# Kernel tuning notes

Hardware: AMD Instinct MI355X
Metric: run time of the kernel (lower is better)

Reference implementation:

```python
import jax, jax.numpy as jnp
import numpy as np

B_SZ, L, D_MODEL, D_STATE, D_CONV, EXPAND = 8, 2048, 512, 16, 4, 2
D_INNER = EXPAND * D_MODEL
DT_RANK = (D_MODEL + 15) // 16  # 32
ENC_IN, MARK_IN, C_OUT, PRED_LEN = 7, 4, 7, 96
IN_SIZE = ENC_IN + MARK_IN


def setup_inputs() -> dict:
    key = jax.random.key(0)
    ks = jax.random.split(key, 16)
    s = 0.02
    inp = {
        "x_enc": jax.random.normal(ks[0], (B_SZ, L, ENC_IN), jnp.float32),
        "x_mark_enc": jax.random.normal(ks[1], (B_SZ, L, MARK_IN), jnp.float32),
        "x_dec": jax.random.normal(ks[2], (B_SZ, PRED_LEN, ENC_IN), jnp.float32),
        "x_mark_dec": jax.random.normal(ks[3], (B_SZ, PRED_LEN, MARK_IN), jnp.float32),
        # input_transform
        "W_in": jax.random.normal(ks[4], (IN_SIZE, D_MODEL), jnp.float32) * s,
        "b_in": jnp.zeros((D_MODEL,), jnp.float32),
        # mamba in_proj (no bias)
        "W_inproj": jax.random.normal(ks[5], (D_MODEL, 2 * D_INNER), jnp.float32) * s,
        # depthwise causal conv
        "conv_w": jax.random.normal(ks[6], (D_INNER, D_CONV), jnp.float32) * s,
        "conv_b": jnp.zeros((D_INNER,), jnp.float32),
        # x_proj -> dt, B, C (no bias)
        "W_xproj": jax.random.normal(ks[7], (D_INNER, DT_RANK + 2 * D_STATE), jnp.float32) * s,
        # dt_proj
        "W_dt": jax.random.normal(ks[8], (DT_RANK, D_INNER), jnp.float32) * s,
        "b_dt": jnp.log(jnp.expm1(jnp.full((D_INNER,), 0.01, jnp.float32))),  # softplus-inv of ~0.01
        # S4D real init
        "A_log": jnp.log(jnp.broadcast_to(jnp.arange(1, D_STATE + 1, dtype=jnp.float32), (D_INNER, D_STATE))),
        "D": jnp.ones((D_INNER,), jnp.float32),
        # out_proj (no bias)
        "W_out": jax.random.normal(ks[9], (D_INNER, D_MODEL), jnp.float32) * s,
        # head
        "W_fc": jax.random.normal(ks[10], (D_MODEL, C_OUT), jnp.float32) * s,
        "b_fc": jnp.zeros((C_OUT,), jnp.float32),
    }
    return inp


def _mamba(x, W_inproj, conv_w, conv_b, W_xproj, W_dt, b_dt, A_log, D, W_out):
    # x: (B, L, d_model)
    xz = x @ W_inproj                      # (B, L, 2*d_inner)
    u, z = jnp.split(xz, 2, axis=-1)       # each (B, L, d_inner)
    # causal depthwise conv over time
    u_t = jnp.transpose(u, (0, 2, 1))      # (B, d_inner, L)
    conv = jax.lax.conv_general_dilated(
        u_t, conv_w[:, None, :], (1,), [(D_CONV - 1, 0)],
        dimension_numbers=("NCH", "OIH", "NCH"), feature_group_count=D_INNER)
    u = jax.nn.silu(jnp.transpose(conv, (0, 2, 1)) + conv_b)  # (B, L, d_inner)

    x_dbl = u @ W_xproj                    # (B, L, dt_rank + 2*d_state)
    dt_lo, Bmat, Cmat = jnp.split(x_dbl, [DT_RANK, DT_RANK + D_STATE], axis=-1)
    dt = jax.nn.softplus(dt_lo @ W_dt + b_dt)  # (B, L, d_inner)
    A = -jnp.exp(A_log)                    # (d_inner, d_state)

    def step(h, inp):
        dt_t, B_t, C_t, u_t = inp          # (B,d_inner),(B,d_state),(B,d_state),(B,d_inner)
        dA = jnp.exp(dt_t[:, :, None] * A)                       # (B, d_inner, d_state)
        dBu = dt_t[:, :, None] * B_t[:, None, :] * u_t[:, :, None]
        h = dA * h + dBu
        y = jnp.einsum("bds,bs->bd", h, C_t) + D * u_t
        return h, y

    h0 = jnp.zeros((x.shape[0], D_INNER, D_STATE), x.dtype)
    xs = (jnp.swapaxes(dt, 0, 1), jnp.swapaxes(Bmat, 0, 1),
          jnp.swapaxes(Cmat, 0, 1), jnp.swapaxes(u, 0, 1))
    _, ys = jax.lax.scan(step, h0, xs)     # ys: (L, B, d_inner)
    y = jnp.swapaxes(ys, 0, 1) * jax.nn.silu(z)
    return y @ W_out                       # (B, L, d_model)


def reference(x_enc, x_mark_enc, x_dec, x_mark_dec, W_in, b_in, W_inproj,
              conv_w, conv_b, W_xproj, W_dt, b_dt, A_log, D, W_out, W_fc, b_fc):
    x = jnp.concatenate([x_enc, x_mark_enc], axis=-1) @ W_in + b_in  # (B, L, d_model)
    x = _mamba(x, W_inproj, conv_w, conv_b, W_xproj, W_dt, b_dt, A_log, D, W_out)
    return x[:, -PRED_LEN:, :] @ W_fc + b_fc  # (B, pred_len, c_out)
```

## Files before the change

### kernel.cpp

```cpp
#include <hip/hip_runtime.h>
#include <math.h>

#define BB 8
#define LL 2048
#define DI 1024
#define NS 16
#define RK 32
#define NI 11
#define PRED 96
#define NC 7

static constexpr size_t OFF_WF   = 0;
static constexpr size_t OFF_BF   = 22528;
static constexpr size_t OFF_A2   = 24576;
static constexpr size_t OFF_WOF  = 40960;
static constexpr size_t OFF_CWT  = 48128;
static constexpr size_t OFF_WXH  = 52224;
static constexpr size_t OFF_WDTH = 84992;
static constexpr size_t OFF_BC   = 101376;
static constexpr size_t OFF_CC   = 363520;
static constexpr size_t OFF_YS   = 625664;
static constexpr size_t OFF_PB   = 1412096;
static constexpr size_t OFF_HB   = 5606400;
static constexpr size_t OFF_UH   = 9800704;
static constexpr size_t OFF_DT   = 18189312;
static constexpr size_t OFF_DLH  = 26577920;
static constexpr size_t OFF_PP   = OFF_PB;
static constexpr size_t OFF_PC   = OFF_PB + 196608;

typedef __attribute__((ext_vector_type(8))) __bf16 bf16x8;
typedef __attribute__((ext_vector_type(8))) _Float16 f16x8;
typedef __attribute__((ext_vector_type(4))) float f32x4;
typedef __attribute__((ext_vector_type(2))) float f32x2;

__device__ __forceinline__ float fexp2(float x) {
#if __has_builtin(__builtin_amdgcn_exp2f)
  return __builtin_amdgcn_exp2f(x);
#else
  return exp2f(x);
#endif
}
__device__ __forceinline__ unsigned short f2bf(float f) {
  unsigned int b = __float_as_uint(f);
  unsigned int r = (b + 0x7fffu + ((b >> 16) & 1u)) >> 16;
  return (unsigned short)r;
}
__device__ __forceinline__ unsigned short f2h_u(float f) {
  union { _Float16 h; unsigned short u; } c;
  c.h = (_Float16)f;
  return c.u;
}
__device__ __forceinline__ float h2f(unsigned short u) {
  union { unsigned short u; _Float16 h; } c;
  c.u = u;
  return (float)c.h;
}
__device__ __forceinline__ float softp(float a) {
  return (a > 15.f) ? a : __logf(1.f + __expf(a));
}
__device__ __forceinline__ f32x2 pk_mul(f32x2 a, f32x2 b) {
  f32x2 d;
  asm("v_pk_mul_f32 %0, %1, %2" : "=v"(d) : "v"(a), "v"(b));
  return d;
}
__device__ __forceinline__ f32x2 pk_fma(f32x2 a, f32x2 b, f32x2 c) {
  asm("v_pk_fma_f32 %0, %1, %2, %0" : "+v"(c) : "v"(a), "v"(b));
  return c;
}
__device__ __forceinline__ void pow16(float e1, float* p) {
  float c2 = e1 * e1, c4 = c2 * c2, c8 = c4 * c4;
  p[0] = e1; p[1] = c2; p[2] = c2 * e1; p[3] = c4;
  p[4] = c4 * e1; p[5] = c4 * c2; p[6] = c4 * p[2]; p[7] = c8;
#pragma unroll
  for (int j = 0; j < 8; ++j) p[8 + j] = c8 * p[j];
}

__global__ __launch_bounds__(256) void k_pre1(
    const float* __restrict__ W_in, const float* __restrict__ b_in,
    const float* __restrict__ W_inproj, const float* __restrict__ conv_w,
    const float* __restrict__ W_xproj, const float* __restrict__ W_dt,
    const float* __restrict__ A_log,
    const float* __restrict__ W_out, const float* __restrict__ W_fc,
    float* __restrict__ ws) {
  int bid = blockIdx.x, tid = threadIdx.x;
  if (bid < 768) {
    int ks = bid / 96;
    int out = (bid % 96) * 256 + tid;
    int r = out >> 11, c = out & 2047;
    int k0 = ks * 64;
    float acc = 0.f;
    for (int k = 0; k < 64; ++k) {
      float a = (r < NI) ? W_in[r * 512 + k0 + k] : b_in[k0 + k];
      acc = fmaf(a, W_inproj[(size_t)(k0 + k) * 2048 + c], acc);
    }
    ws[OFF_PP + (size_t)ks * 24576 + out] = acc;
  } else if (bid < 832) {
    int idx = (bid - 768) * 256 + tid;
    ws[OFF_A2 + idx] = -expf(A_log[idx]) * 1.4426950408889634f;
  } else if (bid < 1056) {
    int lb = bid - 832;
    int ks = lb / 28;
    int out = (lb % 28) * 256 + tid;
    int d = out / NC, cc = out - d * NC;
    int k0 = ks * 64;
    float acc = 0.f;
    for (int k = 0; k < 64; ++k)
      acc = fmaf(W_out[(size_t)d * 512 + k0 + k], W_fc[(k0 + k) * NC + cc], acc);
    ws[OFF_PC + (size_t)ks * 7168 + out] = acc;
  } else if (bid < 1072) {
    int idx = (bid - 1056) * 256 + tid;
    int k = idx >> 10, dd = idx & 1023;
    ws[OFF_CWT + idx] = conv_w[dd * 4 + k];
  } else if (bid < 1328) {
    int idx = (bid - 1072) * 256 + tid;
    int c = idx >> 10, k = idx & 1023;
    unsigned short* wxh = (unsigned short*)(ws + OFF_WXH);
    wxh[idx] = f2bf(W_xproj[(size_t)k * 64 + c]);
  } else {
    int idx = (bid - 1328) * 256 + tid;
    int dd = idx >> 5, k = idx & 31;
    unsigned short* wdh = (unsigned short*)(ws + OFF_WDTH);
    wdh[idx] = f2h_u(W_dt[(size_t)k * DI + dd]);
  }
}

__global__ __launch_bounds__(256) void k_pre2(float* __restrict__ ws) {
  int idx = blockIdx.x * 256 + threadIdx.x;
  if (idx < 24576) {
    float acc = 0.f;
    for (int ks = 0; ks < 8; ++ks) acc += ws[OFF_PP + (size_t)ks * 24576 + idx];
    int r = idx >> 11, c = idx & 2047;
    if (r < NI) ws[OFF_WF + (size_t)r * 2048 + c] = acc;
    else ws[OFF_BF + c] = acc;
  } else {
    int i2 = idx - 24576;
    float acc = 0.f;
    for (int ks = 0; ks < 8; ++ks) acc += ws[OFF_PC + (size_t)ks * 7168 + i2];
    ws[OFF_WOF + i2] = acc;
  }
}

__global__ __launch_bounds__(256) void k_u(
    const float* __restrict__ xe, const float* __restrict__ xm,
    const float* __restrict__ conv_b, float* __restrict__ ws) {
  __shared__ float scat[11][11];
  __shared__ unsigned short sld[8][264];
  int bid = blockIdx.x, tid = threadIdx.x;
  int tg = bid >> 2, dq = bid & 3;
  int d = dq * 256 + tid;
  int b = tg >> 8;
  int t0 = (tg & 255) * 8;
  if (tid < 121) {
    int k = tid / 11, i = tid - k * 11;
    int tp = t0 - 3 + k;
    float v = 0.f;
    if (tp >= 0) v = (i < 7) ? xe[(size_t)(b * LL + tp) * 7 + i]
                             : xm[(size_t)(b * LL + tp) * 4 + (i - 7)];
    scat[k][i] = v;
  }
  __syncthreads();
  float wfv[NI];
#pragma unroll
  for (int i = 0; i < NI; ++i) wfv[i] = ws[OFF_WF + (size_t)i * 2048 + d];
  float bfu = ws[OFF_BF + d];
  float cwv[4];
#pragma unroll
  for (int k = 0; k < 4; ++k) cwv[k] = ws[OFF_CWT + k * 1024 + d];
  float cbv = conv_b[d];
  float xzv[11];
#pragma unroll
  for (int w2 = 0; w2 < 11; ++w2) {
    int tp = t0 - 3 + w2;
    float xz = bfu;
#pragma unroll
    for (int i = 0; i < NI; ++i) xz = fmaf(scat[w2][i], wfv[i], xz);
    xzv[w2] = (tp >= 0) ? xz : 0.f;
  }
#pragma unroll
  for (int tt = 0; tt < 8; ++tt) {
    float acc = cbv;
#pragma unroll
    for (int k = 0; k < 4; ++k) acc = fmaf(cwv[k], xzv[tt + k], acc);
    float uval = acc / (1.f + __expf(-acc));
    sld[tt][tid] = f2bf(uval);
  }
  __syncthreads();
  unsigned short* uhp = (unsigned short*)(ws + OFF_UH);
  int row = tid >> 5, q = tid & 31;
  *(uint4*)(uhp + (size_t)(b * LL + t0 + row) * DI + dq * 256 + q * 8) =
      *(const uint4*)&sld[row][q * 8];
}

__global__ __launch_bounds__(256) void k_proj(float* __restrict__ ws) {
  __shared__ unsigned short su[32][72];
  __shared__ unsigned short sw[64][72];
  __shared__ unsigned short so_dl[32][32];
  __shared__ unsigned short so_b[32][16];
  __shared__ float so_c[32][16];
  const unsigned short* uh  = (const unsigned short*)(ws + OFF_UH);
  const unsigned short* wxh = (const unsigned short*)(ws + OFF_WXH);
  int bid = blockIdx.x, tid = threadIdx.x;
  int r0 = bid * 32;
  int lane = tid & 63, w = tid >> 6;
  int rt = w >> 1, cp = w & 1;
  int srow = tid >> 3, skg = tid & 7;
  const ushort* ub0 = uh + (size_t)(r0 + srow) * DI + skg * 8;
  const ushort* wb0 = wxh + (size_t)srow * DI + skg * 8;
  uint4 ru[2], rw[2][2];
  ru[0]    = *(const uint4*)(ub0);
  rw[0][0] = *(const uint4*)(wb0);
  rw[0][1] = *(const uint4*)(wb0 + (size_t)32 * DI);
  ru[1]    = *(const uint4*)(ub0 + 64);
  rw[1][0] = *(const uint4*)(wb0 + 64);
  rw[1][1] = *(const uint4*)(wb0 + (size_t)32 * DI + 64);
  f32x4 acc[2];
  acc[0] = (f32x4){0.f, 0.f, 0.f, 0.f};
  acc[1] = (f32x4){0.f, 0.f, 0.f, 0.f};
  int arow = rt * 16 + (lane & 15);
  for (int kt = 0; kt < 16; ++kt) {
    int set = kt & 1;
    __syncthreads();
    *(uint4*)&su[srow][skg * 8]      = ru[set];
    *(uint4*)&sw[srow][skg * 8]      = rw[set][0];
    *(uint4*)&sw[srow + 32][skg * 8] = rw[set][1];
    __syncthreads();
    if (kt + 2 < 16) {
      int ko = (kt + 2) * 64;
      ru[set]    = *(const uint4*)(ub0 + ko);
      rw[set][0] = *(const uint4*)(wb0 + ko);
      rw[set][1] = *(const uint4*)(wb0 + (size_t)32 * DI + ko);
    }
#pragma unroll
    for (int ks = 0; ks < 2; ++ks) {
      int koff = ks * 32 + (lane >> 4) * 8;
      bf16x8 av = *(const bf16x8*)&su[arow][koff];
#pragma unroll
      for (int nt = 0; nt < 2; ++nt) {
        bf16x8 bv = *(const bf16x8*)&sw[cp * 32 + nt * 16 + (lane & 15)][koff];
        acc[nt] = __builtin_amdgcn_mfma_f32_16x16x32_bf16(av, bv, acc[nt], 0, 0, 0);
      }
    }
  }
  int orow = rt * 16 + ((lane >> 4) << 2);
  int ocol = lane & 15;
  __syncthreads();
  if (cp == 0) {
#pragma unroll
    for (int reg = 0; reg < 4; ++reg) {
      so_dl[orow + reg][ocol]      = f2h_u(acc[0][reg]);
      so_dl[orow + reg][16 + ocol] = f2h_u(acc[1][reg]);
    }
  } else {
#pragma unroll
    for (int reg = 0; reg < 4; ++reg) {
      so_b[orow + reg][ocol] = f2h_u(acc[0][reg]);
      so_c[orow + reg][ocol] = acc[1][reg];
    }
  }
  __syncthreads();
  unsigned short* dlh = (unsigned short*)(ws + OFF_DLH);
  unsigned short* bh  = (unsigned short*)(ws + OFF_BC);
  if (tid < 128) {
    ((uint4*)(dlh + (size_t)r0 * 32))[tid] = ((const uint4*)so_dl)[tid];
  } else if (tid < 192) {
    int i = tid - 128;
    ((uint4*)(bh + (size_t)r0 * NS))[i] = ((const uint4*)so_b)[i];
  } else {
    int i = tid - 192;
    uint4* cdst = (uint4*)(ws + OFF_CC + (size_t)r0 * NS);
    cdst[i]      = ((const uint4*)so_c)[i];
    cdst[i + 64] = ((const uint4*)so_c)[i + 64];
  }
}

__global__ __launch_bounds__(256) void k_dt(
    const float* __restrict__ b_dt, float* __restrict__ ws) {
  __shared__ _Float16 sdl[64][44];
  __shared__ _Float16 swd[128][44];
  __shared__ unsigned short sst[64][136];
  const unsigned short* dlh = (const unsigned short*)(ws + OFF_DLH);
  const unsigned short* wdh = (const unsigned short*)(ws + OFF_WDTH);
  unsigned short* dtg = (unsigned short*)(ws + OFF_DT);
  int bid = blockIdx.x, tid = threadIdx.x;
  int tgrp = bid >> 3, dgrp = bid & 7;
  int t0 = tgrp * 64, d0 = dgrp * 128;
  {
    int row = tid >> 2, q = tid & 3;
    *(uint4*)&sdl[row][q * 8] = *(const uint4*)&dlh[(size_t)(t0 + row) * 32 + q * 8];
  }
#pragma unroll
  for (int j = 0; j < 2; ++j) {
    int i = j * 256 + tid, row = i >> 2, q = i & 3;
    *(uint4*)&swd[row][q * 8] = *(const uint4*)&wdh[(size_t)(d0 + row) * 32 + q * 8];
  }
  __syncthreads();
  int lane = tid & 63, w = tid >> 6;
  int cl = lane & 15, kg = lane >> 4;
  f16x8 af = *(const f16x8*)&sdl[w * 16 + cl][kg * 8];
#pragma unroll
  for (int dq = 0; dq < 8; ++dq) {
    f16x8 bf8 = *(const f16x8*)&swd[dq * 16 + cl][kg * 8];
    f32x4 a2 = (f32x4){0.f, 0.f, 0.f, 0.f};
    a2 = __builtin_amdgcn_mfma_f32_16x16x32_f16(af, bf8, a2, 0, 0, 0);
    float bdt = b_dt[d0 + dq * 16 + cl];
#pragma unroll
    for (int r = 0; r < 4; ++r)
      sst[w * 16 + kg * 4 + r][dq * 16 + cl] = f2h_u(softp(a2[r] + bdt));
  }
  __syncthreads();
#pragma unroll
  for (int j = 0; j < 4; ++j) {
    int i = j * 256 + tid, row = i >> 4, q = i & 15;
    *(uint4*)(dtg + (size_t)(t0 + row) * DI + d0 + q * 8) =
        *(const uint4*)&sst[row][q * 8];
  }
}

__global__ __launch_bounds__(128) void k_scan1(float* __restrict__ ws) {
  __shared__ float sBB[64][16];
  int ch = blockIdx.x, dgrp = blockIdx.y, b = blockIdx.z;
  int tid = threadIdx.x;
  int d0 = dgrp * 128, t0 = ch * 64;
  size_t row0 = (size_t)b * LL + t0;
  const unsigned short* uh  = (const unsigned short*)(ws + OFF_UH) + row0 * DI + d0 + tid;
  const unsigned short* dtg = (const unsigned short*)(ws + OFF_DT) + row0 * DI + d0 + tid;
  const unsigned short* Bh  = (const unsigned short*)(ws + OFF_BC) + row0 * NS;
  {
    int row = tid >> 1, q = tid & 1;
    uint4 raw = *(const uint4*)(Bh + (size_t)row * NS + q * 8);
    f16x8 hv = *(f16x8*)&raw;
    float4 f0 = {(float)hv[0], (float)hv[1], (float)hv[2], (float)hv[3]};
    float4 f1 = {(float)hv[4], (float)hv[5], (float)hv[6], (float)hv[7]};
    *(float4*)&sBB[row][q * 8]     = f0;
    *(float4*)&sBB[row][q * 8 + 4] = f1;
  }
  __syncthreads();
  int d = d0 + tid;
  float a20 = ws[OFF_A2 + (size_t)d * NS];
  f32x2 h2[8];
#pragma unroll
  for (int j = 0; j < 8; ++j) h2[j] = (f32x2){0.f, 0.f};
  float S = 0.f;
#pragma unroll 4
  for (int t = 0; t < 64; ++t) {
    float dtv = h2f(dtg[(size_t)t * DI]);
    float uv  = __uint_as_float((unsigned)uh[(size_t)t * DI] << 16);
    float dtu = dtv * uv;
    S += dtv;
    float e1 = fexp2(dtv * a20);
    float c2 = e1 * e1, c4 = c2 * c2, c8 = c4 * c4;
    f32x2 c4p = (f32x2){c4, c4}, c8p = (f32x2){c8, c8};
    f32x2 pr0 = (f32x2){e1, c2};
    f32x2 pr1 = pk_mul(pr0, (f32x2){c2, c2});
    f32x2 pr2 = pk_mul(pr0, c4p);
    f32x2 pr3 = pk_mul(pr1, c4p);
    f32x2 pr4 = pk_mul(pr0, c8p);
    f32x2 pr5 = pk_mul(pr1, c8p);
    f32x2 pr6 = pk_mul(pr2, c8p);
    f32x2 pr7 = pk_mul(pr3, c8p);
    f32x2 du2 = (f32x2){dtu, dtu};
    const f32x2* bp = (const f32x2*)&sBB[t][0];
    h2[0] = pk_fma(pr0, h2[0], pk_mul(bp[0], du2));
    h2[1] = pk_fma(pr1, h2[1], pk_mul(bp[1], du2));
    h2[2] = pk_fma(pr2, h2[2], pk_mul(bp[2], du2));
    h2[3] = pk_fma(pr3, h2[3], pk_mul(bp[3], du2));
    h2[4] = pk_fma(pr4, h2[4], pk_mul(bp[4], du2));
    h2[5] = pk_fma(pr5, h2[5], pk_mul(bp[5], du2));
    h2[6] = pk_fma(pr6, h2[6], pk_mul(bp[6], du2));
    h2[7] = pk_fma(pr7, h2[7], pk_mul(bp[7], du2));
  }
  float E1 = fexp2(S * a20);
  ws[OFF_PB + ((size_t)b * 32 + ch) * 1024 + d] = E1;
  unsigned short* hbh = (unsigned short*)(ws + OFF_HB);
  size_t hbase = (((size_t)b * 32 + ch) * NS) * 1024 + d;
#pragma unroll
  for (int s = 0; s < 16; ++s) {
    float hv = (s & 1) ? h2[s >> 1].y : h2[s >> 1].x;
    hbh[hbase + (size_t)s * 1024] = f2h_u(hv);
  }
}

__global__ __launch_bounds__(128) void k_tail(
    const float* __restrict__ Dvec, float* __restrict__ ws) {
  __shared__ unsigned short sdt[64][128];
  __shared__ unsigned short suu[64][128];
  __shared__ float sBB[64][16];
  __shared__ float sCC[64][16];
  int bid = blockIdx.x, tid = threadIdx.x;
  int b = bid >> 4, dgrp = (bid >> 1) & 7, half = bid & 1;
  int d0 = dgrp * 128, t0 = (30 + half) * 64;
  size_t row0 = (size_t)b * LL + t0;
  const unsigned short* uh  = (const unsigned short*)(ws + OFF_UH) + row0 * DI + d0;
  const unsigned short* dtg = (const unsigned short*)(ws + OFF_DT) + row0 * DI + d0;
  const unsigned short* Bh  = (const unsigned short*)(ws + OFF_BC) + row0 * NS;
  const float* Cp = ws + OFF_CC + row0 * NS;
#pragma unroll
  for (int j = 0; j < 8; ++j) {
    int i = j * 128 + tid, row = i >> 4, q = i & 15;
    *(uint4*)&suu[row][q * 8] = *(const uint4*)(uh + (size_t)row * DI + q * 8);
    *(uint4*)&sdt[row][q * 8] = *(const uint4*)(dtg + (size_t)row * DI + q * 8);
  }
#pragma unroll
  for (int j = 0; j < 2; ++j) {
    int i = j * 128 + tid, row = i >> 2, q = i & 3;
    *(float4*)&sCC[row][q * 4] = *(const float4*)&Cp[(size_t)row * NS + q * 4];
  }
  {
    int row = tid >> 1, q = tid & 1;
    uint4 raw = *(const uint4*)(Bh + (size_t)row * NS + q * 8);
    f16x8 hv = *(f16x8*)&raw;
    float4 f0 = {(float)hv[0], (float)hv[1], (float)hv[2], (float)hv[3]};
    float4 f1 = {(float)hv[4], (float)hv[5], (float)hv[6], (float)hv[7]};
    *(float4*)&sBB[row][q * 8]     = f0;
    *(float4*)&sBB[row][q * 8 + 4] = f1;
  }
  int d = d0 + tid;
  float h[16];
#pragma unroll
  for (int s = 0; s < 16; ++s) h[s] = 0.f;
  const unsigned short* hbh = (const unsigned short*)(ws + OFF_HB);
  int nch = 30 + half;
  for (int c = 0; c < nch; ++c) {
    float E1c = ws[OFF_PB + ((size_t)b * 32 + c) * 1024 + d];
    float P[16];
    pow16(E1c, P);
    size_t cb = (((size_t)b * 32 + c) * NS) * 1024 + d;
#pragma unroll
    for (int s = 0; s < 16; ++s)
      h[s] = fmaf(P[s], h[s], h2f(hbh[cb + (size_t)s * 1024]));
  }
  __syncthreads();
  float a20 = ws[OFF_A2 + (size_t)d * NS];
  float Dv = Dvec[d];
  float* ysp = ws + OFF_YS;
  int tstart = half ? 0 : 32;
  for (int t = 0; t < 64; ++t) {
    float dtv = h2f(sdt[t][tid]);
    float uv  = __uint_as_float((unsigned)suu[t][tid] << 16);
    float dtu = dtv * uv;
    float e1 = fexp2(dtv * a20);
    float p[16];
    pow16(e1, p);
    f32x4 b0 = *(const f32x4*)&sBB[t][0];
    f32x4 b1 = *(const f32x4*)&sBB[t][4];
    f32x4 b2 = *(const f32x4*)&sBB[t][8];
    f32x4 b3 = *(const f32x4*)&sBB[t][12];
#pragma unroll
    for (int j = 0; j < 4; ++j) {
      h[j]      = fmaf(p[j],      h[j],      b0[j] * dtu);
      h[j + 4]  = fmaf(p[j + 4],  h[j + 4],  b1[j] * dtu);
      h[j + 8]  = fmaf(p[j + 8],  h[j + 8],  b2[j] * dtu);
      h[j + 12] = fmaf(p[j + 12], h[j + 12], b3[j] * dtu);
    }
    if (t >= tstart) {
      f32x4 c0 = *(const f32x4*)&sCC[t][0];
      f32x4 c1 = *(const f32x4*)&sCC[t][4];
      f32x4 c2 = *(const f32x4*)&sCC[t][8];
      f32x4 c3 = *(const f32x4*)&sCC[t][12];
      float pv = h[0] * c0[0] + h[1] * c0[1] + h[2] * c0[2] + h[3] * c0[3]
               + h[4] * c1[0] + h[5] * c1[1] + h[6] * c1[2] + h[7] * c1[3]
               + h[8] * c2[0] + h[9] * c2[1] + h[10] * c2[2] + h[11] * c2[3]
               + h[12] * c3[0] + h[13] * c3[1] + h[14] * c3[2] + h[15] * c3[3];
      ysp[((size_t)(b * PRED + (t0 + t - (LL - PRED)))) * DI + d] = fmaf(Dv, uv, pv);
    }
  }
}

__global__ __launch_bounds__(256) void k_out(
    const float* __restrict__ xe, const float* __restrict__ xm,
    const float* __restrict__ b_fc, const float* __restrict__ ws,
    float* __restrict__ out) {
  __shared__ float scat[NI];
  __shared__ float sacc[4][NC];
  int bid = blockIdx.x, tid = threadIdx.x;
  int b = bid / PRED, p = bid - b * PRED;
  int t = LL - PRED + p;
  if (tid < NI) scat[tid] = (tid < 7) ? xe[(size_t)(b * LL + t) * 7 + tid]
                                      : xm[(size_t)(b * LL + t) * 4 + (tid - 7)];
  __syncthreads();
  const float* Wf  = ws + OFF_WF;
  const float* bf  = ws + OFF_BF;
  const float* Wof = ws + OFF_WOF;
  const float* ysp = ws + OFF_YS + ((size_t)bid) * DI;
  float acc[NC];
#pragma unroll
  for (int cc = 0; cc < NC; ++cc) acc[cc] = 0.f;
#pragma unroll
  for (int j = 0; j < 4; ++j) {
    int dd = tid + j * 256;
    float zv = bf[DI + dd];
#pragma unroll
    for (int i = 0; i < NI; ++i) zv = fmaf(scat[i], Wf[(size_t)i * 2048 + DI + dd], zv);
    float g = ysp[dd] * (zv / (1.f + __expf(-zv)));
#pragma unroll
    for (int cc = 0; cc < NC; ++cc) acc[cc] = fmaf(g, Wof[dd * NC + cc], acc[cc]);
  }
#pragma unroll
  for (int cc = 0; cc < NC; ++cc) {
    float v = acc[cc];
    for (int off = 32; off > 0; off >>= 1) v += __shfl_down(v, off);
    if ((tid & 63) == 0) sacc[tid >> 6][cc] = v;
  }
  __syncthreads();
  if (tid < NC)
    out[(size_t)bid * NC + tid] =
        sacc[0][tid] + sacc[1][tid] + sacc[2][tid] + sacc[3][tid] + b_fc[tid];
}

extern "C" void kernel_launch(void* const* d_in, const int* in_sizes, int n_in,
                              void* d_out, int out_size, void* d_ws, size_t ws_size,
                              hipStream_t stream) {
  const float* xe    = (const float*)d_in[0];
  const float* xm    = (const float*)d_in[1];
  const float* W_in  = (const float*)d_in[4];
  const float* b_in  = (const float*)d_in[5];
  const float* W_ip  = (const float*)d_in[6];
  const float* cw    = (const float*)d_in[7];
  const float* cb    = (const float*)d_in[8];
  const float* W_xp  = (const float*)d_in[9];
  const float* W_dt  = (const float*)d_in[10];
  const float* b_dt  = (const float*)d_in[11];
  const float* A_log = (const float*)d_in[12];
  const float* Dv    = (const float*)d_in[13];
  const float* W_out = (const float*)d_in[14];
  const float* W_fc  = (const float*)d_in[15];
  const float* b_fc  = (const float*)d_in[16];
  float* ws  = (float*)d_ws;
  float* out = (float*)d_out;

  k_pre1 <<<1456, 256, 0, stream>>>(W_in, b_in, W_ip, cw, W_xp, W_dt, A_log, W_out, W_fc, ws);
  k_pre2 <<<124, 256, 0, stream>>>(ws);
  k_u    <<<8192, 256, 0, stream>>>(xe, xm, cb, ws);
  k_proj <<<512, 256, 0, stream>>>(ws);
  k_dt   <<<2048, 256, 0, stream>>>(b_dt, ws);
  k_scan1<<<dim3(31, 8, 8), 128, 0, stream>>>(ws);
  k_tail <<<128, 128, 0, stream>>>(Dv, ws);
  k_out  <<<BB * PRED, 256, 0, stream>>>(xe, xm, b_fc, ws, out);
}
```

Before: 143.9 us.

## Store dt transposed per channel-chunk and load MFMA operands directly from global

k_dt now writes dt into a per-(batch, channel, chunk) transposed layout, so each scan thread reads its 64 timesteps of dt as contiguous 16-byte vectors instead of strided 2-byte loads. k_scan1 and k_tail are changed to read that layout, and k_tail drops its shared-memory staging of u and dt. Separately, k_proj drops its LDS double-buffered tiling and feeds the MFMAs straight from global loads, removing the barriers. The dt write becomes more scattered, and k_proj gives up LDS reuse of operands shared between waves.

```diff
diff --git a/kernel.cpp b/kernel.cpp
--- a/kernel.cpp
+++ b/kernel.cpp
@@ -23,7 +23,7 @@
 static constexpr size_t OFF_PB   = 1412096;
 static constexpr size_t OFF_HB   = 5606400;
 static constexpr size_t OFF_UH   = 9800704;
-static constexpr size_t OFF_DT   = 18189312;
+static constexpr size_t OFF_DTT  = 18189312;
 static constexpr size_t OFF_DLH  = 26577920;
 static constexpr size_t OFF_PP   = OFF_PB;
 static constexpr size_t OFF_PC   = OFF_PB + 196608;
@@ -192,8 +192,6 @@
 }
 
 __global__ __launch_bounds__(256) void k_proj(float* __restrict__ ws) {
-  __shared__ unsigned short su[32][72];
-  __shared__ unsigned short sw[64][72];
   __shared__ unsigned short so_dl[32][32];
   __shared__ unsigned short so_b[32][16];
   __shared__ float so_c[32][16];
@@ -203,47 +201,25 @@
   int r0 = bid * 32;
   int lane = tid & 63, w = tid >> 6;
   int rt = w >> 1, cp = w & 1;
-  int srow = tid >> 3, skg = tid & 7;
-  const ushort* ub0 = uh + (size_t)(r0 + srow) * DI + skg * 8;
-  const ushort* wb0 = wxh + (size_t)srow * DI + skg * 8;
-  uint4 ru[2], rw[2][2];
-  ru[0]    = *(const uint4*)(ub0);
-  rw[0][0] = *(const uint4*)(wb0);
-  rw[0][1] = *(const uint4*)(wb0 + (size_t)32 * DI);
-  ru[1]    = *(const uint4*)(ub0 + 64);
-  rw[1][0] = *(const uint4*)(wb0 + 64);
-  rw[1][1] = *(const uint4*)(wb0 + (size_t)32 * DI + 64);
+  int arow = rt * 16 + (lane & 15);
+  int kgo = (lane >> 4) * 8;
+  const ushort* ap  = uh + (size_t)(r0 + arow) * DI + kgo;
+  const ushort* bp0 = wxh + (size_t)(cp * 32 + (lane & 15)) * DI + kgo;
+  const ushort* bp1 = bp0 + (size_t)16 * DI;
   f32x4 acc[2];
   acc[0] = (f32x4){0.f, 0.f, 0.f, 0.f};
   acc[1] = (f32x4){0.f, 0.f, 0.f, 0.f};
-  int arow = rt * 16 + (lane & 15);
-  for (int kt = 0; kt < 16; ++kt) {
-    int set = kt & 1;
-    __syncthreads();
-    *(uint4*)&su[srow][skg * 8]      = ru[set];
-    *(uint4*)&sw[srow][skg * 8]      = rw[set][0];
-    *(uint4*)&sw[srow + 32][skg * 8] = rw[set][1];
-    __syncthreads();
-    if (kt + 2 < 16) {
-      int ko = (kt + 2) * 64;
-      ru[set]    = *(const uint4*)(ub0 + ko);
-      rw[set][0] = *(const uint4*)(wb0 + ko);
-      rw[set][1] = *(const uint4*)(wb0 + (size_t)32 * DI + ko);
-    }
-#pragma unroll
-    for (int ks = 0; ks < 2; ++ks) {
-      int koff = ks * 32 + (lane >> 4) * 8;
-      bf16x8 av = *(const bf16x8*)&su[arow][koff];
-#pragma unroll
-      for (int nt = 0; nt < 2; ++nt) {
-        bf16x8 bv = *(const bf16x8*)&sw[cp * 32 + nt * 16 + (lane & 15)][koff];
-        acc[nt] = __builtin_amdgcn_mfma_f32_16x16x32_bf16(av, bv, acc[nt], 0, 0, 0);
-      }
-    }
+#pragma unroll 4
+  for (int kk = 0; kk < 32; ++kk) {
+    int off = kk * 32;
+    bf16x8 av  = *(const bf16x8*)(ap + off);
+    bf16x8 bv0 = *(const bf16x8*)(bp0 + off);
+    bf16x8 bv1 = *(const bf16x8*)(bp1 + off);
+    acc[0] = __builtin_amdgcn_mfma_f32_16x16x32_bf16(av, bv0, acc[0], 0, 0, 0);
+    acc[1] = __builtin_amdgcn_mfma_f32_16x16x32_bf16(av, bv1, acc[1], 0, 0, 0);
   }
   int orow = rt * 16 + ((lane >> 4) << 2);
   int ocol = lane & 15;
-  __syncthreads();
   if (cp == 0) {
 #pragma unroll
     for (int reg = 0; reg < 4; ++reg) {
@@ -277,12 +253,13 @@
     const float* __restrict__ b_dt, float* __restrict__ ws) {
   __shared__ _Float16 sdl[64][44];
   __shared__ _Float16 swd[128][44];
-  __shared__ unsigned short sst[64][136];
+  __shared__ unsigned short sst[128][72];
   const unsigned short* dlh = (const unsigned short*)(ws + OFF_DLH);
   const unsigned short* wdh = (const unsigned short*)(ws + OFF_WDTH);
-  unsigned short* dtg = (unsigned short*)(ws + OFF_DT);
+  unsigned short* dtT = (unsigned short*)(ws + OFF_DTT);
   int bid = blockIdx.x, tid = threadIdx.x;
   int tgrp = bid >> 3, dgrp = bid & 7;
+  int b = tgrp >> 5, ch = tgrp & 31;
   int t0 = tgrp * 64, d0 = dgrp * 128;
   {
     int row = tid >> 2, q = tid & 3;
@@ -305,13 +282,13 @@
     float bdt = b_dt[d0 + dq * 16 + cl];
 #pragma unroll
     for (int r = 0; r < 4; ++r)
-      sst[w * 16 + kg * 4 + r][dq * 16 + cl] = f2h_u(softp(a2[r] + bdt));
+      sst[dq * 16 + cl][w * 16 + kg * 4 + r] = f2h_u(softp(a2[r] + bdt));
   }
   __syncthreads();
 #pragma unroll
   for (int j = 0; j < 4; ++j) {
-    int i = j * 256 + tid, row = i >> 4, q = i & 15;
-    *(uint4*)(dtg + (size_t)(t0 + row) * DI + d0 + q * 8) =
+    int i = j * 256 + tid, row = i >> 3, q = i & 7;
+    *(uint4*)(dtT + (((size_t)(b * DI + d0 + row) * 32 + ch) << 6) + q * 8) =
         *(const uint4*)&sst[row][q * 8];
   }
 }
@@ -322,8 +299,10 @@
   int tid = threadIdx.x;
   int d0 = dgrp * 128, t0 = ch * 64;
   size_t row0 = (size_t)b * LL + t0;
-  const unsigned short* uh  = (const unsigned short*)(ws + OFF_UH) + row0 * DI + d0 + tid;
-  const unsigned short* dtg = (const unsigned short*)(ws + OFF_DT) + row0 * DI + d0 + tid;
+  int d = d0 + tid;
+  const unsigned short* uh  = (const unsigned short*)(ws + OFF_UH) + row0 * DI + d;
+  const uint4* dtp = (const uint4*)((const unsigned short*)(ws + OFF_DTT) +
+                                    (((size_t)(b * DI + d) * 32 + ch) << 6));
   const unsigned short* Bh  = (const unsigned short*)(ws + OFF_BC) + row0 * NS;
   {
     int row = tid >> 1, q = tid & 1;
@@ -335,39 +314,45 @@
     *(float4*)&sBB[row][q * 8 + 4] = f1;
   }
   __syncthreads();
-  int d = d0 + tid;
   float a20 = ws[OFF_A2 + (size_t)d * NS];
   f32x2 h2[8];
 #pragma unroll
   for (int j = 0; j < 8; ++j) h2[j] = (f32x2){0.f, 0.f};
   float S = 0.f;
-#pragma unroll 4
-  for (int t = 0; t < 64; ++t) {
-    float dtv = h2f(dtg[(size_t)t * DI]);
-    float uv  = __uint_as_float((unsigned)uh[(size_t)t * DI] << 16);
-    float dtu = dtv * uv;
-    S += dtv;
-    float e1 = fexp2(dtv * a20);
-    float c2 = e1 * e1, c4 = c2 * c2, c8 = c4 * c4;
-    f32x2 c4p = (f32x2){c4, c4}, c8p = (f32x2){c8, c8};
-    f32x2 pr0 = (f32x2){e1, c2};
-    f32x2 pr1 = pk_mul(pr0, (f32x2){c2, c2});
-    f32x2 pr2 = pk_mul(pr0, c4p);
-    f32x2 pr3 = pk_mul(pr1, c4p);
-    f32x2 pr4 = pk_mul(pr0, c8p);
-    f32x2 pr5 = pk_mul(pr1, c8p);
-    f32x2 pr6 = pk_mul(pr2, c8p);
-    f32x2 pr7 = pk_mul(pr3, c8p);
-    f32x2 du2 = (f32x2){dtu, dtu};
-    const f32x2* bp = (const f32x2*)&sBB[t][0];
-    h2[0] = pk_fma(pr0, h2[0], pk_mul(bp[0], du2));
-    h2[1] = pk_fma(pr1, h2[1], pk_mul(bp[1], du2));
-    h2[2] = pk_fma(pr2, h2[2], pk_mul(bp[2], du2));
-    h2[3] = pk_fma(pr3, h2[3], pk_mul(bp[3], du2));
-    h2[4] = pk_fma(pr4, h2[4], pk_mul(bp[4], du2));
-    h2[5] = pk_fma(pr5, h2[5], pk_mul(bp[5], du2));
-    h2[6] = pk_fma(pr6, h2[6], pk_mul(bp[6], du2));
-    h2[7] = pk_fma(pr7, h2[7], pk_mul(bp[7], du2));
+  for (int g = 0; g < 8; ++g) {
+    uint4 dv = dtp[g];
+    unsigned dw[4] = {dv.x, dv.y, dv.z, dv.w};
+#pragma unroll
+    for (int jj = 0; jj < 8; ++jj) {
+      int t = g * 8 + jj;
+      unsigned short du = (jj & 1) ? (unsigned short)(dw[jj >> 1] >> 16)
+                                   : (unsigned short)(dw[jj >> 1] & 0xffffu);
+      float dtv = h2f(du);
+      float uv  = __uint_as_float((unsigned)uh[(size_t)t * DI] << 16);
+      float dtu = dtv * uv;
+      S += dtv;
+      float e1 = fexp2(dtv * a20);
+      float c2 = e1 * e1, c4 = c2 * c2, c8 = c4 * c4;
+      f32x2 c4p = (f32x2){c4, c4}, c8p = (f32x2){c8, c8};
+      f32x2 pr0 = (f32x2){e1, c2};
+      f32x2 pr1 = pk_mul(pr0, (f32x2){c2, c2});
+      f32x2 pr2 = pk_mul(pr0, c4p);
+      f32x2 pr3 = pk_mul(pr1, c4p);
+      f32x2 pr4 = pk_mul(pr0, c8p);
+      f32x2 pr5 = pk_mul(pr1, c8p);
+      f32x2 pr6 = pk_mul(pr2, c8p);
+      f32x2 pr7 = pk_mul(pr3, c8p);
+      f32x2 du2 = (f32x2){dtu, dtu};
+      const f32x2* bp = (const f32x2*)&sBB[t][0];
+      h2[0] = pk_fma(pr0, h2[0], pk_mul(bp[0], du2));
+      h2[1] = pk_fma(pr1, h2[1], pk_mul(bp[1], du2));
+      h2[2] = pk_fma(pr2, h2[2], pk_mul(bp[2], du2));
+      h2[3] = pk_fma(pr3, h2[3], pk_mul(bp[3], du2));
+      h2[4] = pk_fma(pr4, h2[4], pk_mul(bp[4], du2));
+      h2[5] = pk_fma(pr5, h2[5], pk_mul(bp[5], du2));
+      h2[6] = pk_fma(pr6, h2[6], pk_mul(bp[6], du2));
+      h2[7] = pk_fma(pr7, h2[7], pk_mul(bp[7], du2));
+    }
   }
   float E1 = fexp2(S * a20);
   ws[OFF_PB + ((size_t)b * 32 + ch) * 1024 + d] = E1;
@@ -382,24 +367,18 @@
 
 __global__ __launch_bounds__(128) void k_tail(
     const float* __restrict__ Dvec, float* __restrict__ ws) {
-  __shared__ unsigned short sdt[64][128];
-  __shared__ unsigned short suu[64][128];
   __shared__ float sBB[64][16];
   __shared__ float sCC[64][16];
   int bid = blockIdx.x, tid = threadIdx.x;
   int b = bid >> 4, dgrp = (bid >> 1) & 7, half = bid & 1;
-  int d0 = dgrp * 128, t0 = (30 + half) * 64;
+  int d0 = dgrp * 128, t0 = (30 + half) * 64, ch = 30 + half;
   size_t row0 = (size_t)b * LL + t0;
-  const unsigned short* uh  = (const unsigned short*)(ws + OFF_UH) + row0 * DI + d0;
-  const unsigned short* dtg = (const unsigned short*)(ws + OFF_DT) + row0 * DI + d0;
+  int d = d0 + tid;
+  const unsigned short* uh  = (const unsigned short*)(ws + OFF_UH) + row0 * DI + d;
+  const uint4* dtp = (const uint4*)((const unsigned short*)(ws + OFF_DTT) +
+                                    (((size_t)(b * DI + d) * 32 + ch) << 6));
   const unsigned short* Bh  = (const unsigned short*)(ws + OFF_BC) + row0 * NS;
   const float* Cp = ws + OFF_CC + row0 * NS;
-#pragma unroll
-  for (int j = 0; j < 8; ++j) {
-    int i = j * 128 + tid, row = i >> 4, q = i & 15;
-    *(uint4*)&suu[row][q * 8] = *(const uint4*)(uh + (size_t)row * DI + q * 8);
-    *(uint4*)&sdt[row][q * 8] = *(const uint4*)(dtg + (size_t)row * DI + q * 8);
-  }
 #pragma unroll
   for (int j = 0; j < 2; ++j) {
     int i = j * 128 + tid, row = i >> 2, q = i & 3;
@@ -414,7 +393,6 @@
     *(float4*)&sBB[row][q * 8]     = f0;
     *(float4*)&sBB[row][q * 8 + 4] = f1;
   }
-  int d = d0 + tid;
   float h[16];
 #pragma unroll
   for (int s = 0; s < 16; ++s) h[s] = 0.f;
@@ -434,34 +412,42 @@
   float Dv = Dvec[d];
   float* ysp = ws + OFF_YS;
   int tstart = half ? 0 : 32;
-  for (int t = 0; t < 64; ++t) {
-    float dtv = h2f(sdt[t][tid]);
-    float uv  = __uint_as_float((unsigned)suu[t][tid] << 16);
-    float dtu = dtv * uv;
-    float e1 = fexp2(dtv * a20);
-    float p[16];
-    pow16(e1, p);
-    f32x4 b0 = *(const f32x4*)&sBB[t][0];
-    f32x4 b1 = *(const f32x4*)&sBB[t][4];
-    f32x4 b2 = *(const f32x4*)&sBB[t][8];
-    f32x4 b3 = *(const f32x4*)&sBB[t][12];
-#pragma unroll
-    for (int j = 0; j < 4; ++j) {
-      h[j]      = fmaf(p[j],      h[j],      b0[j] * dtu);
-      h[j + 4]  = fmaf(p[j + 4],  h[j + 4],  b1[j] * dtu);
-      h[j + 8]  = fmaf(p[j + 8],  h[j + 8],  b2[j] * dtu);
-      h[j + 12] = fmaf(p[j + 12], h[j + 12], b3[j] * dtu);
-    }
-    if (t >= tstart) {
-      f32x4 c0 = *(const f32x4*)&sCC[t][0];
-      f32x4 c1 = *(const f32x4*)&sCC[t][4];
-      f32x4 c2 = *(const f32x4*)&sCC[t][8];
-      f32x4 c3 = *(const f32x4*)&sCC[t][12];
-      float pv = h[0] * c0[0] + h[1] * c0[1] + h[2] * c0[2] + h[3] * c0[3]
-               + h[4] * c1[0] + h[5] * c1[1] + h[6] * c1[2] + h[7] * c1[3]
-               + h[8] * c2[0] + h[9] * c2[1] + h[10] * c2[2] + h[11] * c2[3]
-               + h[12] * c3[0] + h[13] * c3[1] + h[14] * c3[2] + h[15] * c3[3];
-      ysp[((size_t)(b * PRED + (t0 + t - (LL - PRED)))) * DI + d] = fmaf(Dv, uv, pv);
+  for (int g = 0; g < 8; ++g) {
+    uint4 dvv = dtp[g];
+    unsigned dw[4] = {dvv.x, dvv.y, dvv.z, dvv.w};
+#pragma unroll
+    for (int jj = 0; jj < 8; ++jj) {
+      int t = g * 8 + jj;
+      unsigned short du = (jj & 1) ? (unsigned short)(dw[jj >> 1] >> 16)
+                                   : (unsigned short)(dw[jj >> 1] & 0xffffu);
+      float dtv = h2f(du);
+      float uv  = __uint_as_float((unsigned)uh[(size_t)t * DI] << 16);
+      float dtu = dtv * uv;
+      float e1 = fexp2(dtv * a20);
+      float p[16];
+      pow16(e1, p);
+      f32x4 b0 = *(const f32x4*)&sBB[t][0];
+      f32x4 b1 = *(const f32x4*)&sBB[t][4];
+      f32x4 b2 = *(const f32x4*)&sBB[t][8];
+      f32x4 b3 = *(const f32x4*)&sBB[t][12];
+#pragma unroll
+      for (int j = 0; j < 4; ++j) {
+        h[j]      = fmaf(p[j],      h[j],      b0[j] * dtu);
+        h[j + 4]  = fmaf(p[j + 4],  h[j + 4],  b1[j] * dtu);
+        h[j + 8]  = fmaf(p[j + 8],  h[j + 8],  b2[j] * dtu);
+        h[j + 12] = fmaf(p[j + 12], h[j + 12], b3[j] * dtu);
+      }
+      if (t >= tstart) {
+        f32x4 c0 = *(const f32x4*)&sCC[t][0];
+        f32x4 c1 = *(const f32x4*)&sCC[t][4];
+        f32x4 c2 = *(const f32x4*)&sCC[t][8];
+        f32x4 c3 = *(const f32x4*)&sCC[t][12];
+        float pv = h[0] * c0[0] + h[1] * c0[1] + h[2] * c0[2] + h[3] * c0[3]
+                 + h[4] * c1[0] + h[5] * c1[1] + h[6] * c1[2] + h[7] * c1[3]
+                 + h[8] * c2[0] + h[9] * c2[1] + h[10] * c2[2] + h[11] * c2[3]
+                 + h[12] * c3[0] + h[13] * c3[1] + h[14] * c3[2] + h[15] * c3[3];
+        ysp[((size_t)(b * PRED + (t0 + t - (LL - PRED)))) * DI + d] = fmaf(Dv, uv, pv);
+      }
     }
   }
 }
```

New measurement: 164.1 us. +14.0%, slower.
